# Kernel optimization log

Measured on AMD Instinct MI355X. Metric: run time of the kernel, lower is better.

## Reference

```python
import jax, jax.numpy as jnp
import numpy as np

K = 3
UP_H, UP_W = 120, 160  # up_size
RES_H, RES_W = UP_H + K - 1, UP_W + K - 1  # bilinear target before valid depthwise conv


def _bilinear_align_corners(x, out_h, out_w):
    """PyTorch UpsamplingBilinear2d (align_corners=True). x: [B,C,H,W]."""
    B, C, H, W = x.shape
    # row interpolation
    hy = jnp.arange(out_h, dtype=x.dtype) * ((H - 1) / (out_h - 1))
    y0 = jnp.floor(hy).astype(jnp.int32)
    y1 = jnp.minimum(y0 + 1, H - 1)
    fy = (hy - y0.astype(x.dtype))[None, None, :, None]
    x = x[:, :, y0, :] * (1 - fy) + x[:, :, y1, :] * fy  # [B,C,out_h,W]
    # col interpolation
    wx = jnp.arange(out_w, dtype=x.dtype) * ((W - 1) / (out_w - 1))
    x0i = jnp.floor(wx).astype(jnp.int32)
    x1i = jnp.minimum(x0i + 1, W - 1)
    fx = (wx - x0i.astype(x.dtype))[None, None, None, :]
    return x[:, :, :, x0i] * (1 - fx) + x[:, :, :, x1i] * fx  # [B,C,out_h,out_w]


def setup_inputs() -> dict:
    key = jax.random.key(0)
    k1, k2, k3 = jax.random.split(key, 3)
    C_in, C_out = 256, 128
    x = jax.random.normal(k1, (8, C_in, 60, 80), dtype=jnp.float32)
    # depthwise kernel [C_in, 1, K, K], pointwise [C_out, C_in]; fan-in-ish scale
    w_dw = jax.random.normal(k2, (C_in, 1, K, K), dtype=jnp.float32) * (1.0 / K)
    w_pw = jax.random.normal(k3, (C_out, C_in), dtype=jnp.float32) * (1.0 / np.sqrt(C_in))
    return {"x": x, "w_dw": w_dw, "w_pw": w_pw}


def reference(x, w_dw, w_pw):
    C_in = x.shape[1]
    # 1) bilinear upsample (align_corners=True) to (UP_H+K-1, UP_W+K-1)
    up = _bilinear_align_corners(x, RES_H, RES_W)
    # 2) depthwise KxK conv, stride 1, VALID padding -> [B,C_in,UP_H,UP_W]
    dw = jax.lax.conv_general_dilated(
        up, w_dw, window_strides=(1, 1), padding="VALID",
        dimension_numbers=("NCHW", "OIHW", "NCHW"),
        feature_group_count=C_in)
    # 3) pointwise 1x1 conv -> [B,C_out,UP_H,UP_W]
    return jnp.einsum("bchw,oc->bohw", dw, w_pw)
```

## Files before the change

kernel.cpp:

```cpp
#include <hip/hip_runtime.h>

#define CIN  256
#define HIN  60
#define WIN  80
#define UPH  120
#define UPW  160
#define COUT 128
#define NPIX (UPH*UPW)

typedef __bf16 bf16x8 __attribute__((ext_vector_type(8)));
typedef float  floatx4 __attribute__((ext_vector_type(4)));

#define A_KC 16
#define A_XR 7
#define A_CP 17
#define A_NT 320

__global__ __launch_bounds__(A_NT, 4) void dw_kernel(
    const float* __restrict__ x,
    const float* __restrict__ wdw,
    __bf16* __restrict__ dwb,
    int b0)
{
    __shared__ float s_x[A_XR * 81 * A_CP];
    __shared__ float s_A[A_KC * 8 * 12];

    const int tid = threadIdx.x;
    const int h0  = blockIdx.x * 8;
    const int cb  = blockIdx.y * A_KC;
    const int bl  = blockIdx.z;
    const int b   = b0 + bl;

    const float HS = 59.0f / 121.0f;
    const float WS = 79.0f / 161.0f;
    const int rbase = (int)(h0 * HS);

    const float* xb = x + ((size_t)b * CIN + cb) * (HIN * WIN);
    #pragma unroll
    for (int it = 0; it < 7; it++) {
        int i = tid + it * A_NT;
        int ch  = i / 140;
        int rem = i - ch * 140;
        int r   = rem / 20;
        int c4  = rem - r * 20;
        int gy  = min(rbase + r, HIN - 1);
        float4 v = *(const float4*)(xb + (size_t)ch * (HIN*WIN) + gy * WIN + c4 * 4);
        int base = (r * 81 + c4 * 4) * A_CP + ch;
        s_x[base]          = v.x;
        s_x[base + A_CP]   = v.y;
        s_x[base + 2*A_CP] = v.z;
        s_x[base + 3*A_CP] = v.w;
    }
    if (tid < A_XR * A_KC) {
        int r = tid / A_KC, ch = tid - r * A_KC;
        s_x[(r * 81 + 80) * A_CP + ch] = 0.f;
    }
    for (int i = tid; i < A_KC * 8 * 9; i += A_NT) {
        int ch  = i / 72;
        int rem = i - ch * 72;
        int h   = rem / 9;
        int dyj = rem - h * 9;
        int dy  = dyj / 3;
        int j   = dyj - dy * 3;
        int ybh = (int)((h0 + h) * HS);
        float acc = 0.f;
        #pragma unroll
        for (int i3 = 0; i3 < 3; i3++) {
            float hy = (h0 + h + i3) * HS;
            int y0 = (int)hy;
            float fy = hy - (float)y0;
            int y1 = min(y0 + 1, HIN - 1);
            float wgt = ((y0 - ybh) == dy ? (1.f - fy) : 0.f)
                      + ((y1 - ybh) == dy ? fy : 0.f);
            acc = fmaf(wgt, wdw[(cb + ch) * 9 + i3 * 3 + j], acc);
        }
        s_A[(ch * 8 + h) * 12 + dy * 4 + j] = acc;
    }
    __syncthreads();

    const int ch = tid & 15;
    const int hg = (tid >> 4) & 1;
    const int ws = tid >> 5;
    int rbh[4];
    #pragma unroll
    for (int hh = 0; hh < 4; hh++)
        rbh[hh] = (int)((h0 + hg * 4 + hh) * HS) - rbase;
    const int rlo = rbh[0];

    #pragma unroll
    for (int k = 0; k < 2; k++) {
        const int w8 = ws + 10 * k;
        const int wq = w8 * 8;
        float fx[10]; int idx[10];
        #pragma unroll
        for (int j = 0; j < 10; j++) {
            float wx = (float)(wq + j) * WS;
            int x0 = (int)wx;
            fx[j]  = wx - (float)x0;
            idx[j] = (rlo * 81 + x0) * A_CP + ch;
        }
        float d[4][8];
        #pragma unroll
        for (int hh = 0; hh < 4; hh++)
            #pragma unroll
            for (int i = 0; i < 8; i++) d[hh][i] = 0.f;

        #pragma unroll
        for (int r = 0; r < 5; r++) {
            const int rabs = rlo + r;
            float cx[10];
            #pragma unroll
            for (int j = 0; j < 10; j++) {
                float a  = s_x[idx[j]];
                float bb = s_x[idx[j] + A_CP];
                cx[j] = fmaf(fx[j], bb - a, a);
                idx[j] += 81 * A_CP;
            }
            #pragma unroll
            for (int hh = 0; hh < 4; hh++) {
                int dyL = rabs - rbh[hh];
                if ((unsigned)dyL <= 2u) {
                    floatx4 Aq = *(const floatx4*)&s_A[(ch * 8 + hg * 4 + hh) * 12 + dyL * 4];
                    #pragma unroll
                    for (int i = 0; i < 8; i++)
                        d[hh][i] = fmaf(Aq[0], cx[i],
                                   fmaf(Aq[1], cx[i+1],
                                   fmaf(Aq[2], cx[i+2], d[hh][i])));
                }
            }
        }
        #pragma unroll
        for (int hh = 0; hh < 4; hh++) {
            bf16x8 o;
            #pragma unroll
            for (int i = 0; i < 8; i++) o[i] = (__bf16)d[hh][i];
            size_t off = ((size_t)bl * CIN + cb + ch) * NPIX
                       + (size_t)(h0 + hg * 4 + hh) * UPW + wq;
            *(bf16x8*)(dwb + off) = o;
        }
    }
}

#define B_NT 512
#define B_WS 264
#define B_DS 40

__global__ __launch_bounds__(B_NT, 4) void pw_kernel(
    const __bf16* __restrict__ dwb,
    const float* __restrict__ wpw,
    float* __restrict__ out,
    int b0)
{
    __shared__ __align__(16) __bf16 s_wpw[COUT * B_WS];
    __shared__ __align__(16) __bf16 s_dw[128 * B_DS];

    const int tid  = threadIdx.x;
    const int tile = blockIdx.x;
    const int bl   = blockIdx.y;
    const int b    = b0 + bl;

    {
        const int o = tid >> 2, seg = tid & 3;
        #pragma unroll
        for (int q = 0; q < 8; q++) {
            int c0 = seg * 64 + q * 8;
            float4 v0 = *(const float4*)(wpw + (size_t)o * CIN + c0);
            float4 v1 = *(const float4*)(wpw + (size_t)o * CIN + c0 + 4);
            bf16x8 f = {(__bf16)v0.x, (__bf16)v0.y, (__bf16)v0.z, (__bf16)v0.w,
                        (__bf16)v1.x, (__bf16)v1.y, (__bf16)v1.z, (__bf16)v1.w};
            *(bf16x8*)&s_wpw[o * B_WS + c0] = f;
        }
    }

    const int wave = tid >> 6, lane = tid & 63;
    const int quad = lane >> 4, l16 = lane & 15;
    const int o32  = (wave & 3) * 32;
    const int pg   = wave >> 2;

    floatx4 acc[2][4];
    #pragma unroll
    for (int a = 0; a < 2; a++)
        #pragma unroll
        for (int p = 0; p < 4; p++) acc[a][p] = (floatx4){0.f,0.f,0.f,0.f};

    const __bf16* dwbase = dwb + (size_t)bl * CIN * NPIX + tile * 128;
    const int cS = tid & 31, p8 = tid >> 5;

    for (int ck = 0; ck < 8; ck++) {
        __syncthreads();
        bf16x8 v = *(const bf16x8*)(dwbase + (size_t)(ck * 32 + cS) * NPIX + p8 * 8);
        #pragma unroll
        for (int i = 0; i < 8; i++)
            s_dw[(p8 * 8 + i) * B_DS + cS] = v[i];
        __syncthreads();

        bf16x8 af0 = *(const bf16x8*)&s_wpw[(o32 + l16) * B_WS + ck * 32 + quad * 8];
        bf16x8 af1 = *(const bf16x8*)&s_wpw[(o32 + 16 + l16) * B_WS + ck * 32 + quad * 8];
        #pragma unroll
        for (int pt = 0; pt < 4; pt++) {
            bf16x8 bf = *(const bf16x8*)&s_dw[(pg * 64 + pt * 16 + l16) * B_DS + quad * 8];
            acc[0][pt] = __builtin_amdgcn_mfma_f32_16x16x32_bf16(af0, bf, acc[0][pt], 0, 0, 0);
            acc[1][pt] = __builtin_amdgcn_mfma_f32_16x16x32_bf16(af1, bf, acc[1][pt], 0, 0, 0);
        }
    }

    float* ob = out + (size_t)b * COUT * NPIX + tile * 128;
    #pragma unroll
    for (int ot = 0; ot < 2; ot++)
        #pragma unroll
        for (int pt = 0; pt < 4; pt++)
            #pragma unroll
            for (int r = 0; r < 4; r++)
                ob[(size_t)(o32 + ot * 16 + quad * 4 + r) * NPIX
                   + pg * 64 + pt * 16 + l16] = acc[ot][pt][r];
}

extern "C" void kernel_launch(void* const* d_in, const int* in_sizes, int n_in,
                              void* d_out, int out_size, void* d_ws, size_t ws_size,
                              hipStream_t stream) {
    const float* x   = (const float*)d_in[0];
    const float* wdw = (const float*)d_in[1];
    const float* wpw = (const float*)d_in[2];
    float* out = (float*)d_out;
    __bf16* dwb = (__bf16*)d_ws;

    int bs = 8;
    while (bs > 1 && (size_t)bs * CIN * NPIX * 2 > ws_size) bs >>= 1;

    for (int b0 = 0; b0 < 8; b0 += bs) {
        dim3 gA(15, CIN / A_KC, bs);
        dw_kernel<<<gA, A_NT, 0, stream>>>(x, wdw, dwb, b0);
        dim3 gB(NPIX / 128, bs);
        pw_kernel<<<gB, B_NT, 0, stream>>>(dwb, wpw, out, b0);
    }
}
```

Measured before the change: 207.4 us.

## Shrink depthwise tiles, pre-pair bf16 neighbours in LDS, prefetch pointwise loads

The depthwise kernel now handles 4 output rows per block instead of 8, which doubles the grid. It stores input pixels in shared memory as bf16 pairs (x0, x0+1), so each horizontal interpolation needs one LDS read instead of two, and occupancy is raised to 5 blocks. The pointwise kernel loads the next channel chunk of depthwise output into a register while the current chunk is being computed. Storing inputs as bf16 lowers interpolation precision, and smaller tiles reload more overlapping halo rows.

Measured after the change: 202.9 us. -2.2%, faster.

```diff
diff --git a/kernel.cpp b/kernel.cpp
--- a/kernel.cpp
+++ b/kernel.cpp
@@ -8,26 +8,27 @@
 #define COUT 128
 #define NPIX (UPH*UPW)
 
+typedef __bf16 bf16x2 __attribute__((ext_vector_type(2)));
 typedef __bf16 bf16x8 __attribute__((ext_vector_type(8)));
 typedef float  floatx4 __attribute__((ext_vector_type(4)));
 
-#define A_KC 16
-#define A_XR 7
+#define A_NT 320
+#define A_XR 5
 #define A_CP 17
-#define A_NT 320
-
-__global__ __launch_bounds__(A_NT, 4) void dw_kernel(
+#define A_AS 49
+
+__global__ __launch_bounds__(A_NT, 5) void dw_kernel(
     const float* __restrict__ x,
     const float* __restrict__ wdw,
     __bf16* __restrict__ dwb,
     int b0)
 {
-    __shared__ float s_x[A_XR * 81 * A_CP];
-    __shared__ float s_A[A_KC * 8 * 12];
+    __shared__ bf16x2 s_px[A_XR * 84 * A_CP];
+    __shared__ float  s_A[16 * A_AS];
 
     const int tid = threadIdx.x;
-    const int h0  = blockIdx.x * 8;
-    const int cb  = blockIdx.y * A_KC;
+    const int h0  = blockIdx.x * 4;
+    const int cb  = blockIdx.y * 16;
     const int bl  = blockIdx.z;
     const int b   = b0 + bl;
 
@@ -37,27 +38,36 @@
 
     const float* xb = x + ((size_t)b * CIN + cb) * (HIN * WIN);
     #pragma unroll
-    for (int it = 0; it < 7; it++) {
-        int i = tid + it * A_NT;
-        int ch  = i / 140;
-        int rem = i - ch * 140;
-        int r   = rem / 20;
-        int c4  = rem - r * 20;
-        int gy  = min(rbase + r, HIN - 1);
-        float4 v = *(const float4*)(xb + (size_t)ch * (HIN*WIN) + gy * WIN + c4 * 4);
-        int base = (r * 81 + c4 * 4) * A_CP + ch;
-        s_x[base]          = v.x;
-        s_x[base + A_CP]   = v.y;
-        s_x[base + 2*A_CP] = v.z;
-        s_x[base + 3*A_CP] = v.w;
-    }
-    if (tid < A_XR * A_KC) {
-        int r = tid / A_KC, ch = tid - r * A_KC;
-        s_x[(r * 81 + 80) * A_CP + ch] = 0.f;
-    }
-    for (int i = tid; i < A_KC * 8 * 9; i += A_NT) {
-        int ch  = i / 72;
-        int rem = i - ch * 72;
+    for (int k = 0; k < 6; k++) {
+        int i = tid + k * A_NT;
+        if (i < 1680) {
+            int ch  = i / 105;
+            int rem = i - ch * 105;
+            int r   = rem / 21;
+            int c4  = rem - r * 21;
+            int gy  = min(rbase + r, HIN - 1);
+            const float* xrow = xb + (size_t)ch * (HIN * WIN) + gy * WIN;
+            int base = (r * 84 + c4 * 4) * A_CP + ch;
+            if (c4 < 20) {
+                float4 v = *(const float4*)(xrow + c4 * 4);
+                float x5 = xrow[min(c4 * 4 + 4, WIN - 1)];
+                s_px[base]          = (bf16x2){(__bf16)v.x, (__bf16)v.y};
+                s_px[base + A_CP]   = (bf16x2){(__bf16)v.y, (__bf16)v.z};
+                s_px[base + 2*A_CP] = (bf16x2){(__bf16)v.z, (__bf16)v.w};
+                s_px[base + 3*A_CP] = (bf16x2){(__bf16)v.w, (__bf16)x5};
+            } else {
+                float v = xrow[WIN - 1];
+                bf16x2 p = {(__bf16)v, (__bf16)v};
+                s_px[base]          = p;
+                s_px[base + A_CP]   = p;
+                s_px[base + 2*A_CP] = p;
+                s_px[base + 3*A_CP] = p;
+            }
+        }
+    }
+    for (int i = tid; i < 16 * 4 * 9; i += A_NT) {
+        int ch  = i / 36;
+        int rem = i - ch * 36;
         int h   = rem / 9;
         int dyj = rem - h * 9;
         int dy  = dyj / 3;
@@ -74,70 +84,64 @@
                       + ((y1 - ybh) == dy ? fy : 0.f);
             acc = fmaf(wgt, wdw[(cb + ch) * 9 + i3 * 3 + j], acc);
         }
-        s_A[(ch * 8 + h) * 12 + dy * 4 + j] = acc;
+        s_A[ch * A_AS + h * 12 + dy * 4 + j] = acc;
     }
     __syncthreads();
 
-    const int ch = tid & 15;
-    const int hg = (tid >> 4) & 1;
-    const int ws = tid >> 5;
+    const int ch  = tid & 15;
+    const int rid = tid >> 4;
+    const int wq  = rid * 8;
     int rbh[4];
     #pragma unroll
     for (int hh = 0; hh < 4; hh++)
-        rbh[hh] = (int)((h0 + hg * 4 + hh) * HS) - rbase;
-    const int rlo = rbh[0];
-
-    #pragma unroll
-    for (int k = 0; k < 2; k++) {
-        const int w8 = ws + 10 * k;
-        const int wq = w8 * 8;
-        float fx[10]; int idx[10];
+        rbh[hh] = (int)((h0 + hh) * HS) - rbase;
+
+    float fx[10]; int wi[10];
+    #pragma unroll
+    for (int j = 0; j < 10; j++) {
+        float wx = (float)(wq + j) * WS;
+        int x0 = (int)wx;
+        fx[j] = wx - (float)x0;
+        wi[j] = x0 * A_CP + ch;
+    }
+
+    float d[4][8];
+    #pragma unroll
+    for (int hh = 0; hh < 4; hh++)
+        #pragma unroll
+        for (int i = 0; i < 8; i++) d[hh][i] = 0.f;
+
+    #pragma unroll
+    for (int r = 0; r < A_XR; r++) {
+        float cx[10];
         #pragma unroll
         for (int j = 0; j < 10; j++) {
-            float wx = (float)(wq + j) * WS;
-            int x0 = (int)wx;
-            fx[j]  = wx - (float)x0;
-            idx[j] = (rlo * 81 + x0) * A_CP + ch;
-        }
-        float d[4][8];
-        #pragma unroll
-        for (int hh = 0; hh < 4; hh++)
-            #pragma unroll
-            for (int i = 0; i < 8; i++) d[hh][i] = 0.f;
-
-        #pragma unroll
-        for (int r = 0; r < 5; r++) {
-            const int rabs = rlo + r;
-            float cx[10];
-            #pragma unroll
-            for (int j = 0; j < 10; j++) {
-                float a  = s_x[idx[j]];
-                float bb = s_x[idx[j] + A_CP];
-                cx[j] = fmaf(fx[j], bb - a, a);
-                idx[j] += 81 * A_CP;
+            bf16x2 p = s_px[r * 84 * A_CP + wi[j]];
+            float lo = (float)p[0], hi = (float)p[1];
+            cx[j] = fmaf(fx[j], hi - lo, lo);
+        }
+        #pragma unroll
+        for (int hh = 0; hh < 4; hh++) {
+            int dyL = r - rbh[hh];
+            if ((unsigned)dyL <= 2u) {
+                const float* Ab = &s_A[ch * A_AS + hh * 12 + dyL * 4];
+                float A0 = Ab[0], A1 = Ab[1], A2 = Ab[2];
+                #pragma unroll
+                for (int i = 0; i < 8; i++)
+                    d[hh][i] = fmaf(A0, cx[i],
+                               fmaf(A1, cx[i+1],
+                               fmaf(A2, cx[i+2], d[hh][i])));
             }
-            #pragma unroll
-            for (int hh = 0; hh < 4; hh++) {
-                int dyL = rabs - rbh[hh];
-                if ((unsigned)dyL <= 2u) {
-                    floatx4 Aq = *(const floatx4*)&s_A[(ch * 8 + hg * 4 + hh) * 12 + dyL * 4];
-                    #pragma unroll
-                    for (int i = 0; i < 8; i++)
-                        d[hh][i] = fmaf(Aq[0], cx[i],
-                                   fmaf(Aq[1], cx[i+1],
-                                   fmaf(Aq[2], cx[i+2], d[hh][i])));
-                }
-            }
-        }
-        #pragma unroll
-        for (int hh = 0; hh < 4; hh++) {
-            bf16x8 o;
-            #pragma unroll
-            for (int i = 0; i < 8; i++) o[i] = (__bf16)d[hh][i];
-            size_t off = ((size_t)bl * CIN + cb + ch) * NPIX
-                       + (size_t)(h0 + hg * 4 + hh) * UPW + wq;
-            *(bf16x8*)(dwb + off) = o;
-        }
+        }
+    }
+    #pragma unroll
+    for (int hh = 0; hh < 4; hh++) {
+        bf16x8 o;
+        #pragma unroll
+        for (int i = 0; i < 8; i++) o[i] = (__bf16)d[hh][i];
+        size_t off = ((size_t)bl * CIN + cb + ch) * NPIX
+                   + (size_t)(h0 + hh) * UPW + wq;
+        *(bf16x8*)(dwb + off) = o;
     }
 }
 
@@ -186,13 +190,17 @@
     const __bf16* dwbase = dwb + (size_t)bl * CIN * NPIX + tile * 128;
     const int cS = tid & 31, p8 = tid >> 5;
 
+    bf16x8 v = *(const bf16x8*)(dwbase + (size_t)cS * NPIX + p8 * 8);
+
     for (int ck = 0; ck < 8; ck++) {
         __syncthreads();
-        bf16x8 v = *(const bf16x8*)(dwbase + (size_t)(ck * 32 + cS) * NPIX + p8 * 8);
         #pragma unroll
         for (int i = 0; i < 8; i++)
             s_dw[(p8 * 8 + i) * B_DS + cS] = v[i];
         __syncthreads();
+
+        if (ck < 7)
+            v = *(const bf16x8*)(dwbase + (size_t)((ck+1) * 32 + cS) * NPIX + p8 * 8);
 
         bf16x8 af0 = *(const bf16x8*)&s_wpw[(o32 + l16) * B_WS + ck * 32 + quad * 8];
         bf16x8 af1 = *(const bf16x8*)&s_wpw[(o32 + 16 + l16) * B_WS + ck * 32 + quad * 8];
@@ -228,7 +236,7 @@
     while (bs > 1 && (size_t)bs * CIN * NPIX * 2 > ws_size) bs >>= 1;
 
     for (int b0 = 0; b0 < 8; b0 += bs) {
-        dim3 gA(15, CIN / A_KC, bs);
+        dim3 gA(30, CIN / 16, bs);
         dw_kernel<<<gA, A_NT, 0, stream>>>(x, wdw, dwb, b0);
         dim3 gB(NPIX / 128, bs);
         pw_kernel<<<gB, B_NT, 0, stream>>>(dwb, wpw, out, b0);
```
